# Optimization experiments

Measured on AMD Instinct MI355X. Metric: run time of the kernel, lower is better.

The kernel has to match this reference:

```python
import jax, jax.numpy as jnp
import numpy as np

B, C, D, L, H = 128, 1000, 300, 40, 100


def setup_inputs() -> dict:
    key = jax.random.key(0)
    ks = jax.random.split(key, 16)
    def rn(i, shape, sc=1.0):
        return (jax.random.normal(ks[i], shape, jnp.float32) * sc).astype(jnp.float32)
    return {
        "utt": rn(0, (B, L, D)),
        "sys_slots": rn(1, (B, D), 0.1),
        "conf_slots": rn(2, (B, D), 0.1),
        "conf_values": rn(3, (B, D), 0.1),
        "y_past_state": jax.random.uniform(ks[4], (B, C), jnp.float32),
        "slot_emb": rn(5, (C, D), 0.1),
        "value_emb": rn(6, (C, D), 0.1),
        "Wc": rn(7, (D, 2 * D), 0.05), "bc": jnp.zeros((D,), jnp.float32),
        "conv_w1": rn(8, (D, D, 1), 0.05), "conv_b1": jnp.zeros((D,), jnp.float32),
        "conv_w2": rn(9, (D, D, 2), 0.05), "conv_b2": jnp.zeros((D,), jnp.float32),
        "conv_w3": rn(10, (D, D, 3), 0.05), "conv_b3": jnp.zeros((D,), jnp.float32),
        "Wd": rn(11, (H, D), 0.05), "bd": jnp.zeros((H,), jnp.float32),
        "Wmr": rn(12, (H, D), 0.05), "bmr": jnp.zeros((H,), jnp.float32),
        "Wmc": rn(13, (H, D), 0.05), "bmc": jnp.zeros((H,), jnp.float32),
        "Wj": rn(14, (1, H), 0.05), "bj": jnp.zeros((1,), jnp.float32),
    }


def _conv_relu_pool(x_ncl, w, b):
    # x_ncl: [B, D, L]; w: [F, D, k] -> relu(conv) then global max-pool over time -> [B, F]
    y = jax.lax.conv_general_dilated(x_ncl, w, (1,), 'VALID',
                                     dimension_numbers=('NCH', 'OIH', 'NCH'))
    y = jax.nn.relu(y + b[None, :, None])
    return jnp.max(y, axis=2)


def _sig_linear(x, W, b):
    # Sequential(Sigmoid, Linear): Linear applied to sigmoid(x)
    return jax.nn.sigmoid(x) @ W.T + b


def reference(utt, sys_slots, conf_slots, conf_values, y_past_state,
              slot_emb, value_emb, Wc, bc,
              conv_w1, conv_b1, conv_w2, conv_b2, conv_w3, conv_b3,
              Wd, bd, Wmr, bmr, Wmc, bmc, Wj, bj):
    # CNN utterance encoder: sum of 3 conv branches (filter widths 1,2,3)
    x = jnp.transpose(utt, (0, 2, 1))  # [B, D, L]
    final_utt = (_conv_relu_pool(x, conv_w1, conv_b1)
                 + _conv_relu_pool(x, conv_w2, conv_b2)
                 + _conv_relu_pool(x, conv_w3, conv_b3))  # [B, D]

    # candidates_transform = sigmoid(Linear(cat(slot_emb, value_emb)))
    cand = jax.nn.sigmoid(jnp.concatenate([slot_emb, value_emb], axis=1) @ Wc.T + bc)  # [C, D]

    # fused version of the per-batch repeat/addcmul loop: [B, C, D]
    contrib = cand[None, :, :] * final_utt[:, None, :]

    y1 = _sig_linear(_sig_linear(contrib, Wd, bd), Wj, bj)  # [B, C, 1]

    # system-act request gate: ([C,D]@[D,B]) @ [B,D] -> [C, D]
    m_r = (slot_emb @ sys_slots.T) @ final_utt
    y2 = _sig_linear(_sig_linear(m_r, Wmr, bmr), Wj, bj)  # [C, 1]

    # system-act confirm gate
    m_c = ((slot_emb @ conf_slots.T) * (value_emb @ conf_values.T)) @ final_utt  # [C, D]
    y3 = _sig_linear(_sig_linear(m_c, Wmc, bmc), Wj, bj)  # [C, 1]

    y_presoftmax = y1 + y2[None, :, :] + y3[None, :, :]  # [B, C, 1]
    combine = 0.5
    return combine * y_presoftmax[..., 0] + (1.0 - combine) * y_past_state  # [B, C]
```

## Files before the change

### kernel.cpp

```cpp
#include <hip/hip_runtime.h>
#include <hip/hip_bf16.h>

#define OFF_Y23     0
#define OFF_BDP     4096
#define OFF_WJP     4544
#define OFF_BCP     4992
#define OFF_BMRP    6272
#define OFF_BMCP    6720
#define OFF_WALLT   7168
#define OFF_PBF     1235968
#define OFF_FUBF    20896768
#define OFF_FUBFT   20978688
#define OFF_CATSV   21060608
#define OFF_WCPK    22371328
#define OFF_CANDBF  22780928
#define OFF_WDFRAG  23436288
#define OFF_WMRFRAG 23507968
#define OFF_WMCFRAG 23579648
#define OFF_SYSB    23651328
#define OFF_CONFSB  23733248
#define OFF_CONFVB  23815168
#define OFF_PRBF    23897088
#define OFF_PCBF    24159232
#define OFF_SMRBF   24421376
#define OFF_SMCBF   25076736
#define OFF_XBF     25732096

typedef short bf16x8_t __attribute__((ext_vector_type(8)));
typedef float f32x4_t  __attribute__((ext_vector_type(4)));

__device__ __forceinline__ float sigmoidf_fast(float x) {
    return __builtin_amdgcn_rcpf(1.0f + __expf(-x));
}
__device__ __forceinline__ unsigned short f2bf(float x) {
    unsigned int u = __float_as_uint(x);
    unsigned int r = (u + 0x7FFFu + ((u >> 16) & 1u)) >> 16;
    return (unsigned short)r;
}
__device__ __forceinline__ float bf2f(unsigned short h) {
    return __uint_as_float(((unsigned int)h) << 16);
}

__global__ __launch_bounds__(256) void pack_kernel(const float* __restrict__ w1,
        const float* __restrict__ w2, const float* __restrict__ w3,
        const float* __restrict__ Wc, const float* __restrict__ Wd,
        const float* __restrict__ Wmr, const float* __restrict__ Wmc,
        const float* __restrict__ sys, const float* __restrict__ confs,
        const float* __restrict__ confv, const float* __restrict__ bd,
        const float* __restrict__ Wj, const float* __restrict__ bmr,
        const float* __restrict__ bmc, const float* __restrict__ bc,
        const float* __restrict__ slot, const float* __restrict__ value,
        const float* __restrict__ utt,
        unsigned short* __restrict__ WallTbf, unsigned short* __restrict__ WdFrag,
        unsigned short* __restrict__ WmrFrag, unsigned short* __restrict__ WmcFrag,
        float* __restrict__ bdPad, float* __restrict__ WjPad,
        float* __restrict__ bmrPad, float* __restrict__ bmcPad,
        float* __restrict__ bcPad,
        unsigned short* __restrict__ sysB, unsigned short* __restrict__ confsB,
        unsigned short* __restrict__ confvB, unsigned short* __restrict__ catsv,
        unsigned short* __restrict__ WcPk, unsigned short* __restrict__ Xbf) {
    int t = blockIdx.x * 256 + threadIdx.x;
    union { unsigned short u[8]; uint4 q; } o;
    if (t < 76800) {
        int i8 = t * 8;
        int tap = i8 / 102400;
        int rem = i8 - tap * 102400;
        int f = rem / 320, k0 = rem % 320;
        #pragma unroll
        for (int e = 0; e < 8; e++) {
            int k = k0 + e;
            float v = 0.0f;
            if (f < 300 && k < 300) {
                int fd = f * 300 + k;
                v = (tap == 0) ? w1[fd] : (tap == 1) ? w2[fd * 2]
                  : (tap == 2) ? w2[fd * 2 + 1] : w3[fd * 3 + (tap - 3)];
            }
            o.u[e] = f2bf(v);
        }
        *(uint4*)(WallTbf + i8) = o.q;
    } else if (t < 90240) {
        int ent = t - 76800;
        int mat = ent / 4480;
        int le = ent - mat * 4480;
        const float* W = (mat == 0) ? Wd : ((mat == 1) ? Wmr : Wmc);
        unsigned short* dst = (mat == 0) ? WdFrag : ((mat == 1) ? WmrFrag : WmcFrag);
        int kt = le / 448;
        int r = le - kt * 448;
        int ni = r >> 6, lane = r & 63;
        int j = ni * 16 + (lane & 15);
        int kb = kt * 32 + (lane >> 4) * 8;
        #pragma unroll
        for (int e = 0; e < 8; e++) {
            int k = kb + e;
            o.u[e] = f2bf((j < 100 && k < 300) ? W[j * 300 + k] : 0.0f);
        }
        *(uint4*)(dst + le * 8) = o.q;
    } else if (t < 105600) {
        int i8 = (t - 90240) * 8;
        int m = i8 / 40960, r = i8 - m * 40960;
        int bb = r / 320, k0 = r % 320;
        const float* src = (m == 0) ? sys : ((m == 1) ? confs : confv);
        unsigned short* dst = (m == 0) ? sysB : ((m == 1) ? confsB : confvB);
        #pragma unroll
        for (int e = 0; e < 8; e++) {
            int k = k0 + e;
            o.u[e] = f2bf((k < 300) ? src[bb * 300 + k] : 0.0f);
        }
        *(uint4*)(dst + r) = o.q;
    } else if (t < 187520) {
        int i8 = (t - 105600) * 8;
        int c = i8 / 640, k0 = i8 % 640;
        #pragma unroll
        for (int e = 0; e < 8; e++) {
            int k = k0 + e;
            float v = 0.0f;
            if (c < 1000) {
                if (k < 300)                  v = slot[c * 300 + k];
                else if (k >= 320 && k < 620) v = value[c * 300 + (k - 320)];
            }
            o.u[e] = f2bf(v);
        }
        *(uint4*)(catsv + i8) = o.q;
    } else if (t < 213120) {
        int i8 = (t - 187520) * 8;
        int f = i8 / 640, k0 = i8 % 640;
        #pragma unroll
        for (int e = 0; e < 8; e++) {
            int k = k0 + e;
            float v = 0.0f;
            if (f < 300) {
                if (k < 300)                  v = Wc[f * 600 + k];
                else if (k >= 320 && k < 620) v = Wc[f * 600 + 300 + (k - 320)];
            }
            o.u[e] = f2bf(v);
        }
        *(uint4*)(WcPk + i8) = o.q;
    } else if (t < 417920) {
        int i8 = (t - 213120) * 8;
        int m = i8 / 320, k0 = i8 % 320;
        if (k0 + 8 <= 300) {
            float4 a = *(const float4*)(utt + m * 300 + k0);
            float4 b = *(const float4*)(utt + m * 300 + k0 + 4);
            o.u[0] = f2bf(a.x); o.u[1] = f2bf(a.y); o.u[2] = f2bf(a.z); o.u[3] = f2bf(a.w);
            o.u[4] = f2bf(b.x); o.u[5] = f2bf(b.y); o.u[6] = f2bf(b.z); o.u[7] = f2bf(b.w);
        } else {
            #pragma unroll
            for (int e = 0; e < 8; e++) {
                int k = k0 + e;
                o.u[e] = f2bf((k < 300) ? utt[m * 300 + k] : 0.0f);
            }
        }
        *(uint4*)(Xbf + i8) = o.q;
    } else if (t < 418688) {
        int j = t - 417920;
        if (j < 112)      bdPad[j] = (j < 100) ? bd[j] : 0.0f;
        else if (j < 224) { int jj = j - 112; WjPad[jj]  = (jj < 100) ? Wj[jj]  : 0.0f; }
        else if (j < 336) { int jj = j - 224; bmrPad[jj] = (jj < 100) ? bmr[jj] : 0.0f; }
        else if (j < 448) { int jj = j - 336; bmcPad[jj] = (jj < 100) ? bmc[jj] : 0.0f; }
        else              { int jj = j - 448; bcPad[jj]  = (jj < 300) ? bc[jj]  : 0.0f; }
    }
}

__global__ __launch_bounds__(256, 4) void early_kernel(
        const unsigned short* __restrict__ Xbf, const unsigned short* __restrict__ WallTbf,
        unsigned short* __restrict__ Pbf,
        const unsigned short* __restrict__ catsv, const unsigned short* __restrict__ WcPk,
        const float* __restrict__ bcPad, unsigned short* __restrict__ candbf,
        const unsigned short* __restrict__ sysB, const unsigned short* __restrict__ confsB,
        const unsigned short* __restrict__ confvB,
        unsigned short* __restrict__ Prbf, unsigned short* __restrict__ Pcbf) {
    __shared__ __attribute__((aligned(16))) char smem[25600];
    const int bid = blockIdx.x;
    const int tid = threadIdx.x;
    const int lane = tid & 63, w = tid >> 6;
    const int ln = lane & 15, lq = lane >> 4;

    if (bid >= 112) {
        short* As = (short*)smem;
        short* Bs = (short*)(smem + 5120);
        const int g = bid - 112;
        const int xcd = g & 7;
        const int idx2 = g >> 3;
        const int m0 = (xcd * 10 + idx2 / 15) * 64;
        const int n0 = (idx2 % 15) * 128;
        const int arow = tid >> 2, aq = tid & 3;
        f32x4_t acc[4][2];
        #pragma unroll
        for (int i = 0; i < 4; i++)
            #pragma unroll
            for (int j = 0; j < 2; j++) acc[i][j] = (f32x4_t){0.f, 0.f, 0.f, 0.f};

        const unsigned short* aSrc  = Xbf + (m0 + arow) * 320 + aq * 8;
        const unsigned short* bSrc0 = WallTbf + (n0 + arow) * 320 + aq * 8;
        const unsigned short* bSrc1 = WallTbf + (n0 + 64 + arow) * 320 + aq * 8;
        uint4 pa  = *(const uint4*)(aSrc);
        uint4 pb0 = *(const uint4*)(bSrc0);
        uint4 pb1 = *(const uint4*)(bSrc1);
        *(uint4*)(&As[arow * 40 + aq * 8]) = pa;
        *(uint4*)(&Bs[arow * 40 + aq * 8]) = pb0;
        *(uint4*)(&Bs[(64 + arow) * 40 + aq * 8]) = pb1;
        __syncthreads();

        #pragma unroll 1
        for (int kt = 0; kt < 10; kt++) {
            if (kt < 9) {
                int kk2 = (kt + 1) * 32;
                pa  = *(const uint4*)(aSrc + kk2);
                pb0 = *(const uint4*)(bSrc0 + kk2);
                pb1 = *(const uint4*)(bSrc1 + kk2);
            }
            bf16x8_t a[4], b[2];
            #pragma unroll
            for (int mi = 0; mi < 4; mi++)
                a[mi] = *(const bf16x8_t*)(&As[(mi * 16 + ln) * 40 + lq * 8]);
            #pragma unroll
            for (int ni = 0; ni < 2; ni++)
                b[ni] = *(const bf16x8_t*)(&Bs[(w * 32 + ni * 16 + ln) * 40 + lq * 8]);
            #pragma unroll
            for (int mi = 0; mi < 4; mi++)
                #pragma unroll
                for (int ni = 0; ni < 2; ni++)
                    acc[mi][ni] = __builtin_amdgcn_mfma_f32_16x16x32_bf16(a[mi], b[ni], acc[mi][ni], 0, 0, 0);
            if (kt < 9) {
                __syncthreads();
                *(uint4*)(&As[arow * 40 + aq * 8]) = pa;
                *(uint4*)(&Bs[arow * 40 + aq * 8]) = pb0;
                *(uint4*)(&Bs[(64 + arow) * 40 + aq * 8]) = pb1;
                __syncthreads();
            }
        }
        #pragma unroll
        for (int mi = 0; mi < 4; mi++) {
            #pragma unroll
            for (int ni = 0; ni < 2; ni++) {
                int col = n0 + w * 32 + ni * 16 + ln;
                #pragma unroll
                for (int reg = 0; reg < 4; reg++) {
                    int row = m0 + mi * 16 + lq * 4 + reg;
                    Pbf[row * 1920 + col] = f2bf(acc[mi][ni][reg]);
                }
            }
        }
    } else if (bid < 80) {
        short* As = (short*)smem;
        short* Bs = (short*)(smem + 5120);
        const int m0 = (bid / 5) * 64, n0 = (bid % 5) * 64;
        const int wr = w & 1, wc = w >> 1;
        f32x4_t acc[2][2];
        #pragma unroll
        for (int i = 0; i < 2; i++)
            #pragma unroll
            for (int j = 0; j < 2; j++) acc[i][j] = (f32x4_t){0.f, 0.f, 0.f, 0.f};
        const int srow = tid >> 2, sq = tid & 3;
        for (int kk = 0; kk < 640; kk += 32) {
            *(uint4*)(&As[srow * 40 + sq * 8]) = *(const uint4*)(catsv + (m0 + srow) * 640 + kk + sq * 8);
            *(uint4*)(&Bs[srow * 40 + sq * 8]) = *(const uint4*)(WcPk  + (n0 + srow) * 640 + kk + sq * 8);
            __syncthreads();
            bf16x8_t a[2], b[2];
            #pragma unroll
            for (int mi = 0; mi < 2; mi++)
                a[mi] = *(const bf16x8_t*)(&As[(wr * 32 + mi * 16 + ln) * 40 + lq * 8]);
            #pragma unroll
            for (int ni = 0; ni < 2; ni++)
                b[ni] = *(const bf16x8_t*)(&Bs[(wc * 32 + ni * 16 + ln) * 40 + lq * 8]);
            #pragma unroll
            for (int mi = 0; mi < 2; mi++)
                #pragma unroll
                for (int ni = 0; ni < 2; ni++)
                    acc[mi][ni] = __builtin_amdgcn_mfma_f32_16x16x32_bf16(a[mi], b[ni], acc[mi][ni], 0, 0, 0);
            __syncthreads();
        }
        #pragma unroll
        for (int mi = 0; mi < 2; mi++) {
            #pragma unroll
            for (int ni = 0; ni < 2; ni++) {
                int n = n0 + wc * 32 + ni * 16 + ln;
                float bcv = bcPad[n];
                #pragma unroll
                for (int reg = 0; reg < 4; reg++) {
                    int cr = m0 + wr * 32 + mi * 16 + lq * 4 + reg;
                    candbf[cr * 320 + n] = f2bf(sigmoidf_fast(acc[mi][ni][reg] + bcv));
                }
            }
        }
    } else {
        short* As0 = (short*)smem;
        short* As1 = (short*)(smem + 5120);
        short* Bs0 = (short*)(smem + 10240);
        short* Bs1 = (short*)(smem + 15360);
        short* Bs2 = (short*)(smem + 20480);
        const int pid = bid - 80;
        const int c0 = (pid >> 1) * 64;
        const int bh = (pid & 1) * 64;
        f32x4_t accR[4], accS[4], accV[4];
        #pragma unroll
        for (int i = 0; i < 4; i++) {
            accR[i] = (f32x4_t){0.f, 0.f, 0.f, 0.f};
            accS[i] = (f32x4_t){0.f, 0.f, 0.f, 0.f};
            accV[i] = (f32x4_t){0.f, 0.f, 0.f, 0.f};
        }
        for (int kk = 0; kk < 320; kk += 32) {
            #pragma unroll
            for (int i = tid; i < 512; i += 256) {
                int mat = i >> 8, r2 = i & 255;
                int row = r2 >> 2, q = r2 & 3;
                short* dst = mat ? As1 : As0;
                *(uint4*)(&dst[row * 40 + q * 8]) =
                    *(const uint4*)(catsv + (c0 + row) * 640 + mat * 320 + kk + q * 8);
            }
            #pragma unroll
            for (int i = tid; i < 768; i += 256) {
                int mat = i >> 8, r2 = i & 255;
                int row = r2 >> 2, q = r2 & 3;
                const unsigned short* src = (mat == 0) ? sysB : ((mat == 1) ? confsB : confvB);
                short* dst = (mat == 0) ? Bs0 : ((mat == 1) ? Bs1 : Bs2);
                *(uint4*)(&dst[row * 40 + q * 8]) =
                    *(const uint4*)(src + (bh + row) * 320 + kk + q * 8);
            }
            __syncthreads();
            bf16x8_t aS = *(const bf16x8_t*)(&As0[(w * 16 + ln) * 40 + lq * 8]);
            bf16x8_t aV = *(const bf16x8_t*)(&As1[(w * 16 + ln) * 40 + lq * 8]);
            #pragma unroll
            for (int ni = 0; ni < 4; ni++) {
                bf16x8_t bR = *(const bf16x8_t*)(&Bs0[(ni * 16 + ln) * 40 + lq * 8]);
                bf16x8_t bS = *(const bf16x8_t*)(&Bs1[(ni * 16 + ln) * 40 + lq * 8]);
                bf16x8_t bV = *(const bf16x8_t*)(&Bs2[(ni * 16 + ln) * 40 + lq * 8]);
                accR[ni] = __builtin_amdgcn_mfma_f32_16x16x32_bf16(aS, bR, accR[ni], 0, 0, 0);
                accS[ni] = __builtin_amdgcn_mfma_f32_16x16x32_bf16(aS, bS, accS[ni], 0, 0, 0);
                accV[ni] = __builtin_amdgcn_mfma_f32_16x16x32_bf16(aV, bV, accV[ni], 0, 0, 0);
            }
            __syncthreads();
        }
        #pragma unroll
        for (int ni = 0; ni < 4; ni++) {
            int b = bh + ni * 16 + ln;
            #pragma unroll
            for (int reg = 0; reg < 4; reg++) {
                int c = c0 + w * 16 + lq * 4 + reg;
                Prbf[c * 128 + b] = f2bf(accR[ni][reg]);
                Pcbf[c * 128 + b] = f2bf(accS[ni][reg] * accV[ni][reg]);
            }
        }
    }
}

__global__ __launch_bounds__(64) void combine_kernel(const unsigned short* __restrict__ Pbf,
        const float* __restrict__ b1, const float* __restrict__ b2,
        const float* __restrict__ b3, unsigned short* __restrict__ fubf,
        unsigned short* __restrict__ fubfT) {
    int b = blockIdx.x;
    int f = blockIdx.y * 64 + threadIdx.x;
    if (f >= 300) { fubf[b * 320 + f] = 0; fubfT[f * 128 + b] = 0; return; }
    const unsigned short* base = Pbf + (size_t)b * 40 * 1920;
    float m1 = -1e30f, m2 = -1e30f, m3 = -1e30f;
    float p1prev = 0.f, p3prev = 0.f, p3prev2 = 0.f, p4prev = 0.f;
    for (int t = 0; t < 40; ++t) {
        const unsigned short* r = base + t * 1920;
        float p0 = bf2f(r[f]);
        float p1 = bf2f(r[320 + f]);
        float p2 = bf2f(r[640 + f]);
        float p3 = bf2f(r[960 + f]);
        float p4 = bf2f(r[1280 + f]);
        float p5 = bf2f(r[1600 + f]);
        m1 = fmaxf(m1, p0);
        if (t >= 1) m2 = fmaxf(m2, p1prev + p2);
        if (t >= 2) m3 = fmaxf(m3, p3prev2 + p4prev + p5);
        p3prev2 = p3prev; p3prev = p3; p4prev = p4; p1prev = p1;
    }
    float r = fmaxf(m1 + b1[f], 0.f) + fmaxf(m2 + b2[f], 0.f) + fmaxf(m3 + b3[f], 0.f);
    unsigned short rb = f2bf(r);
    fubf[b * 320 + f]  = rb;
    fubfT[f * 128 + b] = rb;
}

__global__ __launch_bounds__(256) void mgate_gemm(const unsigned short* __restrict__ Prbf,
        const unsigned short* __restrict__ Pcbf, const unsigned short* __restrict__ fubfT,
        unsigned short* __restrict__ smrbf, unsigned short* __restrict__ smcbf) {
    __shared__ __attribute__((aligned(16))) short As[2][64 * 40];
    __shared__ __attribute__((aligned(16))) short Bs[64 * 40];
    const int tid = threadIdx.x;
    const int m0 = blockIdx.x * 64, n0 = blockIdx.y * 64;
    const int lane = tid & 63, w = tid >> 6;
    const int wr = w & 1, wc = w >> 1;
    const int ln = lane & 15, lq = lane >> 4;
    f32x4_t accR[2][2], accC[2][2];
    #pragma unroll
    for (int i = 0; i < 2; i++)
        #pragma unroll
        for (int j = 0; j < 2; j++) {
            accR[i][j] = (f32x4_t){0.f, 0.f, 0.f, 0.f};
            accC[i][j] = (f32x4_t){0.f, 0.f, 0.f, 0.f};
        }
    for (int kk = 0; kk < 128; kk += 32) {
        #pragma unroll
        for (int i = tid; i < 512; i += 256) {
            int mat = i >> 8, r2 = i & 255;
            int row = r2 >> 2, q = r2 & 3;
            const unsigned short* src = mat ? Pcbf : Prbf;
            *(uint4*)(&As[mat][row * 40 + q * 8]) =
                *(const uint4*)(src + (m0 + row) * 128 + kk + q * 8);
        }
        if (tid < 256) {
            int row = tid >> 2, q = tid & 3;
            *(uint4*)(&Bs[row * 40 + q * 8]) =
                *(const uint4*)(fubfT + (n0 + row) * 128 + kk + q * 8);
        }
        __syncthreads();
        bf16x8_t aR[2], aC[2], b[2];
        #pragma unroll
        for (int mi = 0; mi < 2; mi++) {
            aR[mi] = *(const bf16x8_t*)(&As[0][(wr * 32 + mi * 16 + ln) * 40 + lq * 8]);
            aC[mi] = *(const bf16x8_t*)(&As[1][(wr * 32 + mi * 16 + ln) * 40 + lq * 8]);
        }
        #pragma unroll
        for (int ni = 0; ni < 2; ni++)
            b[ni] = *(const bf16x8_t*)(&Bs[(wc * 32 + ni * 16 + ln) * 40 + lq * 8]);
        #pragma unroll
        for (int mi = 0; mi < 2; mi++)
            #pragma unroll
            for (int ni = 0; ni < 2; ni++) {
                accR[mi][ni] = __builtin_amdgcn_mfma_f32_16x16x32_bf16(aR[mi], b[ni], accR[mi][ni], 0, 0, 0);
                accC[mi][ni] = __builtin_amdgcn_mfma_f32_16x16x32_bf16(aC[mi], b[ni], accC[mi][ni], 0, 0, 0);
            }
        __syncthreads();
    }
    #pragma unroll
    for (int mi = 0; mi < 2; mi++) {
        #pragma unroll
        for (int ni = 0; ni < 2; ni++) {
            int f = n0 + wc * 32 + ni * 16 + ln;
            #pragma unroll
            for (int reg = 0; reg < 4; reg++) {
                int c = m0 + wr * 32 + mi * 16 + lq * 4 + reg;
                smrbf[c * 320 + f] = f2bf(sigmoidf_fast(accR[mi][ni][reg]));
                smcbf[c * 320 + f] = f2bf(sigmoidf_fast(accC[mi][ni][reg]));
            }
        }
    }
}

__global__ __launch_bounds__(256) void ygate_gemm(const unsigned short* __restrict__ smrbf,
        const unsigned short* __restrict__ smcbf, const unsigned short* __restrict__ WmrFrag,
        const unsigned short* __restrict__ WmcFrag, const float* __restrict__ bmrPad,
        const float* __restrict__ bmcPad, const float* __restrict__ WjPad,
        const float* __restrict__ bj, float* __restrict__ y23) {
    __shared__ __attribute__((aligned(16))) short As[2][64 * 40];
    __shared__ __attribute__((aligned(16))) short Bs[2][3584];
    const int tid = threadIdx.x;
    const int c0 = blockIdx.x * 64;
    const int lane = tid & 63, w = tid >> 6;
    const int ln = lane & 15, lq = lane >> 4;
    f32x4_t accR[7], accC[7];
    #pragma unroll
    for (int i = 0; i < 7; i++) {
        accR[i] = (f32x4_t){0.f, 0.f, 0.f, 0.f};
        accC[i] = (f32x4_t){0.f, 0.f, 0.f, 0.f};
    }
    for (int kt = 0; kt < 10; kt++) {
        int kk = kt * 32;
        #pragma unroll
        for (int i = tid; i < 512; i += 256) {
            int mat = i >> 8, r2 = i & 255;
            int row = r2 >> 2, q = r2 & 3;
            const unsigned short* src = mat ? smcbf : smrbf;
            *(uint4*)(&As[mat][row * 40 + q * 8]) =
                *(const uint4*)(src + (c0 + row) * 320 + kk + q * 8);
        }
        #pragma unroll
        for (int i = tid; i < 896; i += 256) {
            int mat = i / 448, j = i - mat * 448;
            const uint4* s = (const uint4*)((mat ? WmcFrag : WmrFrag) + kt * 3584);
            ((uint4*)&Bs[mat][0])[j] = s[j];
        }
        __syncthreads();
        bf16x8_t aR = *(const bf16x8_t*)(&As[0][(w * 16 + ln) * 40 + lq * 8]);
        bf16x8_t aC = *(const bf16x8_t*)(&As[1][(w * 16 + ln) * 40 + lq * 8]);
        #pragma unroll
        for (int ni = 0; ni < 7; ni++) {
            bf16x8_t bR = *(const bf16x8_t*)(&Bs[0][(ni * 64 + lane) * 8]);
            bf16x8_t bC = *(const bf16x8_t*)(&Bs[1][(ni * 64 + lane) * 8]);
            accR[ni] = __builtin_amdgcn_mfma_f32_16x16x32_bf16(aR, bR, accR[ni], 0, 0, 0);
            accC[ni] = __builtin_amdgcn_mfma_f32_16x16x32_bf16(aC, bC, accC[ni], 0, 0, 0);
        }
        __syncthreads();
    }
    float psum[4] = {0.f, 0.f, 0.f, 0.f};
    #pragma unroll
    for (int ni = 0; ni < 7; ni++) {
        int n = ni * 16 + ln;
        float wj = WjPad[n], br = bmrPad[n], bcv = bmcPad[n];
        #pragma unroll
        for (int reg = 0; reg < 4; reg++) {
            float hr = sigmoidf_fast(accR[ni][reg] + br);
            float hc = sigmoidf_fast(accC[ni][reg] + bcv);
            psum[reg] += (hr + hc) * wj;
        }
    }
    #pragma unroll
    for (int reg = 0; reg < 4; reg++) {
        float v = psum[reg];
        v += __shfl_xor(v, 1);
        v += __shfl_xor(v, 2);
        v += __shfl_xor(v, 4);
        v += __shfl_xor(v, 8);
        if (ln == 0) {
            int c = c0 + w * 16 + lq * 4 + reg;
            y23[c] = v + 2.0f * bj[0];
        }
    }
}

__global__ __launch_bounds__(256) void gemm2_kernel(const unsigned short* __restrict__ candbf,
        const unsigned short* __restrict__ fubf, const unsigned short* __restrict__ WdFrag,
        const float* __restrict__ bdPad, const float* __restrict__ WjPad,
        const float* __restrict__ bj, const float* __restrict__ y23,
        const float* __restrict__ ypast, float* __restrict__ out) {
    __shared__ __attribute__((aligned(16))) short Bs[2][3584];
    __shared__ float bdS[112], WjS[112], ybuf[128];
    const int c = blockIdx.x;
    const int tid = threadIdx.x;
    const int lane = tid & 63, w = tid >> 6;
    const int ln = lane & 15, lq = lane >> 4;
    if (tid < 112) { bdS[tid] = bdPad[tid]; WjS[tid] = WjPad[tid]; }

    const unsigned short* candRow = candbf + c * 320;
    const unsigned short* fuR0 = fubf + (w * 32 + ln) * 320;
    const unsigned short* fuR1 = fuR0 + 16 * 320;

    f32x4_t acc[2][7];
    #pragma unroll
    for (int mi = 0; mi < 2; mi++)
        #pragma unroll
        for (int ni = 0; ni < 7; ni++) acc[mi][ni] = (f32x4_t){0.f, 0.f, 0.f, 0.f};

    {
        const uint4* src = (const uint4*)(WdFrag);
        uint4* dst = (uint4*)&Bs[0][0];
        dst[tid] = src[tid];
        if (tid < 192) dst[tid + 256] = src[tid + 256];
    }
    __syncthreads();

    #pragma unroll
    for (int kt = 0; kt < 10; kt++) {
        if (kt < 9) {
            const uint4* src = (const uint4*)(WdFrag + (kt + 1) * 3584);
            uint4* dst = (uint4*)&Bs[(kt + 1) & 1][0];
            dst[tid] = src[tid];
            if (tid < 192) dst[tid + 256] = src[tid + 256];
        }
        const int k0 = kt * 32 + lq * 8;
        bf16x8_t cf  = *(const bf16x8_t*)(candRow + k0);
        bf16x8_t f0v = *(const bf16x8_t*)(fuR0 + k0);
        bf16x8_t f1v = *(const bf16x8_t*)(fuR1 + k0);
        bf16x8_t a0, a1;
        #pragma unroll
        for (int e = 0; e < 8; e += 2) {
            float cv0 = bf2f((unsigned short)cf[e]);
            float cv1 = bf2f((unsigned short)cf[e + 1]);
            float2 s0 = make_float2(sigmoidf_fast(cv0 * bf2f((unsigned short)f0v[e])),
                                    sigmoidf_fast(cv1 * bf2f((unsigned short)f0v[e + 1])));
            float2 s1 = make_float2(sigmoidf_fast(cv0 * bf2f((unsigned short)f1v[e])),
                                    sigmoidf_fast(cv1 * bf2f((unsigned short)f1v[e + 1])));
            __hip_bfloat162 p0 = __float22bfloat162_rn(s0);
            __hip_bfloat162 p1 = __float22bfloat162_rn(s1);
            ((unsigned int*)&a0)[e >> 1] = *(unsigned int*)&p0;
            ((unsigned int*)&a1)[e >> 1] = *(unsigned int*)&p1;
        }
        #pragma unroll
        for (int ni = 0; ni < 7; ni++) {
            bf16x8_t bfr = *(const bf16x8_t*)(&Bs[kt & 1][(ni * 64 + lane) * 8]);
            acc[0][ni] = __builtin_amdgcn_mfma_f32_16x16x32_bf16(a0, bfr, acc[0][ni], 0, 0, 0);
            acc[1][ni] = __builtin_amdgcn_mfma_f32_16x16x32_bf16(a1, bfr, acc[1][ni], 0, 0, 0);
        }
        __syncthreads();
    }

    float psum[2][4] = {{0.f, 0.f, 0.f, 0.f}, {0.f, 0.f, 0.f, 0.f}};
    #pragma unroll
    for (int mi = 0; mi < 2; mi++) {
        #pragma unroll
        for (int ni = 0; ni < 7; ni++) {
            int n = ni * 16 + ln;
            float bdv = bdS[n], wjv = WjS[n];
            #pragma unroll
            for (int reg = 0; reg < 4; reg++) {
                float h = sigmoidf_fast(acc[mi][ni][reg] + bdv);
                psum[mi][reg] += h * wjv;
            }
        }
    }
    #pragma unroll
    for (int mi = 0; mi < 2; mi++) {
        #pragma unroll
        for (int reg = 0; reg < 4; reg++) {
            float v = psum[mi][reg];
            v += __shfl_xor(v, 1);
            v += __shfl_xor(v, 2);
            v += __shfl_xor(v, 4);
            v += __shfl_xor(v, 8);
            if (ln == 0) ybuf[w * 32 + mi * 16 + lq * 4 + reg] = v;
        }
    }
    __syncthreads();
    if (tid < 128) {
        int b = tid;
        float y1 = ybuf[b] + bj[0];
        out[b * 1000 + c] = 0.5f * (y1 + y23[c]) + 0.5f * ypast[b * 1000 + c];
    }
}

extern "C" void kernel_launch(void* const* d_in, const int* in_sizes, int n_in,
                              void* d_out, int out_size, void* d_ws, size_t ws_size,
                              hipStream_t stream) {
    const float* utt   = (const float*)d_in[0];
    const float* sys   = (const float*)d_in[1];
    const float* confs = (const float*)d_in[2];
    const float* confv = (const float*)d_in[3];
    const float* ypast = (const float*)d_in[4];
    const float* slot  = (const float*)d_in[5];
    const float* value = (const float*)d_in[6];
    const float* Wc    = (const float*)d_in[7];
    const float* bc    = (const float*)d_in[8];
    const float* w1    = (const float*)d_in[9];
    const float* b1    = (const float*)d_in[10];
    const float* w2    = (const float*)d_in[11];
    const float* b2    = (const float*)d_in[12];
    const float* w3    = (const float*)d_in[13];
    const float* b3    = (const float*)d_in[14];
    const float* Wd    = (const float*)d_in[15];
    const float* bd    = (const float*)d_in[16];
    const float* Wmr   = (const float*)d_in[17];
    const float* bmr   = (const float*)d_in[18];
    const float* Wmc   = (const float*)d_in[19];
    const float* bmc   = (const float*)d_in[20];
    const float* Wj    = (const float*)d_in[21];
    const float* bj    = (const float*)d_in[22];

    char* wsb = (char*)d_ws;
    float* y23    = (float*)(wsb + OFF_Y23);
    float* bdPad  = (float*)(wsb + OFF_BDP);
    float* WjPad  = (float*)(wsb + OFF_WJP);
    float* bcPad  = (float*)(wsb + OFF_BCP);
    float* bmrPad = (float*)(wsb + OFF_BMRP);
    float* bmcPad = (float*)(wsb + OFF_BMCP);
    unsigned short* WallTbf = (unsigned short*)(wsb + OFF_WALLT);
    unsigned short* Pbf     = (unsigned short*)(wsb + OFF_PBF);
    unsigned short* fubf    = (unsigned short*)(wsb + OFF_FUBF);
    unsigned short* fubfT   = (unsigned short*)(wsb + OFF_FUBFT);
    unsigned short* catsv   = (unsigned short*)(wsb + OFF_CATSV);
    unsigned short* WcPk    = (unsigned short*)(wsb + OFF_WCPK);
    unsigned short* candbf  = (unsigned short*)(wsb + OFF_CANDBF);
    unsigned short* WdFrag  = (unsigned short*)(wsb + OFF_WDFRAG);
    unsigned short* WmrFrag = (unsigned short*)(wsb + OFF_WMRFRAG);
    unsigned short* WmcFrag = (unsigned short*)(wsb + OFF_WMCFRAG);
    unsigned short* sysB    = (unsigned short*)(wsb + OFF_SYSB);
    unsigned short* confsB  = (unsigned short*)(wsb + OFF_CONFSB);
    unsigned short* confvB  = (unsigned short*)(wsb + OFF_CONFVB);
    unsigned short* Prbf    = (unsigned short*)(wsb + OFF_PRBF);
    unsigned short* Pcbf    = (unsigned short*)(wsb + OFF_PCBF);
    unsigned short* smrbf   = (unsigned short*)(wsb + OFF_SMRBF);
    unsigned short* smcbf   = (unsigned short*)(wsb + OFF_SMCBF);
    unsigned short* Xbf     = (unsigned short*)(wsb + OFF_XBF);
    float* out = (float*)d_out;

    pack_kernel<<<1636, 256, 0, stream>>>(w1, w2, w3, Wc, Wd, Wmr, Wmc, sys, confs, confv,
                                          bd, Wj, bmr, bmc, bc, slot, value, utt,
                                          WallTbf, WdFrag, WmrFrag, WmcFrag,
                                          bdPad, WjPad, bmrPad, bmcPad, bcPad,
                                          sysB, confsB, confvB, catsv, WcPk, Xbf);
    early_kernel<<<1312, 256, 0, stream>>>(Xbf, WallTbf, Pbf,
                                           catsv, WcPk, bcPad, candbf,
                                           sysB, confsB, confvB, Prbf, Pcbf);
    combine_kernel<<<dim3(128, 5), 64, 0, stream>>>(Pbf, b1, b2, b3, fubf, fubfT);
    mgate_gemm<<<dim3(16, 5), 256, 0, stream>>>(Prbf, Pcbf, fubfT, smrbf, smcbf);
    ygate_gemm<<<16, 256, 0, stream>>>(smrbf, smcbf, WmrFrag, WmcFrag,
                                       bmrPad, bmcPad, WjPad, bj, y23);
    gemm2_kernel<<<1000, 256, 0, stream>>>(candbf, fubf, WdFrag, bdPad, WjPad,
                                           bj, y23, ypast, out);
}
```

Baseline: 191.5 us.

## Load MFMA operands directly from global memory, dropping LDS staging and barriers

In three GEMM kernels (mgate_gemm, ygate_gemm, gemm2_kernel), the shared-memory staging of A/B tiles is removed and each lane loads its bf16x8 MFMA fragments straight from global memory, relying on L1/L2 caching. All __syncthreads in the k-loops go away, and gemm2 gets a launch_bounds occupancy hint of 4 plus partial unrolling. This removes LDS copy traffic and barrier stalls, but can raise global/L2 load traffic, since tiles are no longer shared across waves, and exposes load latency without explicit double-buffering.

```diff
diff --git a/kernel.cpp b/kernel.cpp
--- a/kernel.cpp
+++ b/kernel.cpp
@@ -376,8 +376,6 @@
 __global__ __launch_bounds__(256) void mgate_gemm(const unsigned short* __restrict__ Prbf,
         const unsigned short* __restrict__ Pcbf, const unsigned short* __restrict__ fubfT,
         unsigned short* __restrict__ smrbf, unsigned short* __restrict__ smcbf) {
-    __shared__ __attribute__((aligned(16))) short As[2][64 * 40];
-    __shared__ __attribute__((aligned(16))) short Bs[64 * 40];
     const int tid = threadIdx.x;
     const int m0 = blockIdx.x * 64, n0 = blockIdx.y * 64;
     const int lane = tid & 63, w = tid >> 6;
@@ -391,30 +389,18 @@
             accR[i][j] = (f32x4_t){0.f, 0.f, 0.f, 0.f};
             accC[i][j] = (f32x4_t){0.f, 0.f, 0.f, 0.f};
         }
+    #pragma unroll
     for (int kk = 0; kk < 128; kk += 32) {
-        #pragma unroll
-        for (int i = tid; i < 512; i += 256) {
-            int mat = i >> 8, r2 = i & 255;
-            int row = r2 >> 2, q = r2 & 3;
-            const unsigned short* src = mat ? Pcbf : Prbf;
-            *(uint4*)(&As[mat][row * 40 + q * 8]) =
-                *(const uint4*)(src + (m0 + row) * 128 + kk + q * 8);
-        }
-        if (tid < 256) {
-            int row = tid >> 2, q = tid & 3;
-            *(uint4*)(&Bs[row * 40 + q * 8]) =
-                *(const uint4*)(fubfT + (n0 + row) * 128 + kk + q * 8);
-        }
-        __syncthreads();
         bf16x8_t aR[2], aC[2], b[2];
         #pragma unroll
         for (int mi = 0; mi < 2; mi++) {
-            aR[mi] = *(const bf16x8_t*)(&As[0][(wr * 32 + mi * 16 + ln) * 40 + lq * 8]);
-            aC[mi] = *(const bf16x8_t*)(&As[1][(wr * 32 + mi * 16 + ln) * 40 + lq * 8]);
+            int row = m0 + wr * 32 + mi * 16 + ln;
+            aR[mi] = *(const bf16x8_t*)(Prbf + row * 128 + kk + lq * 8);
+            aC[mi] = *(const bf16x8_t*)(Pcbf + row * 128 + kk + lq * 8);
         }
         #pragma unroll
         for (int ni = 0; ni < 2; ni++)
-            b[ni] = *(const bf16x8_t*)(&Bs[(wc * 32 + ni * 16 + ln) * 40 + lq * 8]);
+            b[ni] = *(const bf16x8_t*)(fubfT + (n0 + wc * 32 + ni * 16 + ln) * 128 + kk + lq * 8);
         #pragma unroll
         for (int mi = 0; mi < 2; mi++)
             #pragma unroll
@@ -422,7 +408,6 @@
                 accR[mi][ni] = __builtin_amdgcn_mfma_f32_16x16x32_bf16(aR[mi], b[ni], accR[mi][ni], 0, 0, 0);
                 accC[mi][ni] = __builtin_amdgcn_mfma_f32_16x16x32_bf16(aC[mi], b[ni], accC[mi][ni], 0, 0, 0);
             }
-        __syncthreads();
     }
     #pragma unroll
     for (int mi = 0; mi < 2; mi++) {
@@ -444,8 +429,6 @@
         const unsigned short* __restrict__ WmcFrag, const float* __restrict__ bmrPad,
         const float* __restrict__ bmcPad, const float* __restrict__ WjPad,
         const float* __restrict__ bj, float* __restrict__ y23) {
-    __shared__ __attribute__((aligned(16))) short As[2][64 * 40];
-    __shared__ __attribute__((aligned(16))) short Bs[2][3584];
     const int tid = threadIdx.x;
     const int c0 = blockIdx.x * 64;
     const int lane = tid & 63, w = tid >> 6;
@@ -456,33 +439,19 @@
         accR[i] = (f32x4_t){0.f, 0.f, 0.f, 0.f};
         accC[i] = (f32x4_t){0.f, 0.f, 0.f, 0.f};
     }
+    const int arow = (c0 + w * 16 + ln) * 320 + lq * 8;
+    const int bbase = lane * 8;
+    #pragma unroll 2
     for (int kt = 0; kt < 10; kt++) {
-        int kk = kt * 32;
-        #pragma unroll
-        for (int i = tid; i < 512; i += 256) {
-            int mat = i >> 8, r2 = i & 255;
-            int row = r2 >> 2, q = r2 & 3;
-            const unsigned short* src = mat ? smcbf : smrbf;
-            *(uint4*)(&As[mat][row * 40 + q * 8]) =
-                *(const uint4*)(src + (c0 + row) * 320 + kk + q * 8);
-        }
-        #pragma unroll
-        for (int i = tid; i < 896; i += 256) {
-            int mat = i / 448, j = i - mat * 448;
-            const uint4* s = (const uint4*)((mat ? WmcFrag : WmrFrag) + kt * 3584);
-            ((uint4*)&Bs[mat][0])[j] = s[j];
-        }
-        __syncthreads();
-        bf16x8_t aR = *(const bf16x8_t*)(&As[0][(w * 16 + ln) * 40 + lq * 8]);
-        bf16x8_t aC = *(const bf16x8_t*)(&As[1][(w * 16 + ln) * 40 + lq * 8]);
+        bf16x8_t aR = *(const bf16x8_t*)(smrbf + arow + kt * 32);
+        bf16x8_t aC = *(const bf16x8_t*)(smcbf + arow + kt * 32);
         #pragma unroll
         for (int ni = 0; ni < 7; ni++) {
-            bf16x8_t bR = *(const bf16x8_t*)(&Bs[0][(ni * 64 + lane) * 8]);
-            bf16x8_t bC = *(const bf16x8_t*)(&Bs[1][(ni * 64 + lane) * 8]);
+            bf16x8_t bR = *(const bf16x8_t*)(WmrFrag + kt * 3584 + ni * 512 + bbase);
+            bf16x8_t bC = *(const bf16x8_t*)(WmcFrag + kt * 3584 + ni * 512 + bbase);
             accR[ni] = __builtin_amdgcn_mfma_f32_16x16x32_bf16(aR, bR, accR[ni], 0, 0, 0);
             accC[ni] = __builtin_amdgcn_mfma_f32_16x16x32_bf16(aC, bC, accC[ni], 0, 0, 0);
         }
-        __syncthreads();
     }
     float psum[4] = {0.f, 0.f, 0.f, 0.f};
     #pragma unroll
@@ -510,22 +479,21 @@
     }
 }
 
-__global__ __launch_bounds__(256) void gemm2_kernel(const unsigned short* __restrict__ candbf,
+__global__ __launch_bounds__(256, 4) void gemm2_kernel(const unsigned short* __restrict__ candbf,
         const unsigned short* __restrict__ fubf, const unsigned short* __restrict__ WdFrag,
         const float* __restrict__ bdPad, const float* __restrict__ WjPad,
         const float* __restrict__ bj, const float* __restrict__ y23,
         const float* __restrict__ ypast, float* __restrict__ out) {
-    __shared__ __attribute__((aligned(16))) short Bs[2][3584];
-    __shared__ float bdS[112], WjS[112], ybuf[128];
+    __shared__ float ybuf[128];
     const int c = blockIdx.x;
     const int tid = threadIdx.x;
     const int lane = tid & 63, w = tid >> 6;
     const int ln = lane & 15, lq = lane >> 4;
-    if (tid < 112) { bdS[tid] = bdPad[tid]; WjS[tid] = WjPad[tid]; }
 
     const unsigned short* candRow = candbf + c * 320;
     const unsigned short* fuR0 = fubf + (w * 32 + ln) * 320;
     const unsigned short* fuR1 = fuR0 + 16 * 320;
+    const unsigned short* bBase = WdFrag + lane * 8;
 
     f32x4_t acc[2][7];
     #pragma unroll
@@ -533,22 +501,8 @@
         #pragma unroll
         for (int ni = 0; ni < 7; ni++) acc[mi][ni] = (f32x4_t){0.f, 0.f, 0.f, 0.f};
 
-    {
-        const uint4* src = (const uint4*)(WdFrag);
-        uint4* dst = (uint4*)&Bs[0][0];
-        dst[tid] = src[tid];
-        if (tid < 192) dst[tid + 256] = src[tid + 256];
-    }
-    __syncthreads();
-
-    #pragma unroll
+    #pragma unroll 2
     for (int kt = 0; kt < 10; kt++) {
-        if (kt < 9) {
-            const uint4* src = (const uint4*)(WdFrag + (kt + 1) * 3584);
-            uint4* dst = (uint4*)&Bs[(kt + 1) & 1][0];
-            dst[tid] = src[tid];
-            if (tid < 192) dst[tid + 256] = src[tid + 256];
-        }
         const int k0 = kt * 32 + lq * 8;
         bf16x8_t cf  = *(const bf16x8_t*)(candRow + k0);
         bf16x8_t f0v = *(const bf16x8_t*)(fuR0 + k0);
@@ -567,13 +521,13 @@
             ((unsigned int*)&a0)[e >> 1] = *(unsigned int*)&p0;
             ((unsigned int*)&a1)[e >> 1] = *(unsigned int*)&p1;
         }
+        const unsigned short* bkt = bBase + kt * 3584;
         #pragma unroll
         for (int ni = 0; ni < 7; ni++) {
-            bf16x8_t bfr = *(const bf16x8_t*)(&Bs[kt & 1][(ni * 64 + lane) * 8]);
+            bf16x8_t bfr = *(const bf16x8_t*)(bkt + ni * 512);
             acc[0][ni] = __builtin_amdgcn_mfma_f32_16x16x32_bf16(a0, bfr, acc[0][ni], 0, 0, 0);
             acc[1][ni] = __builtin_amdgcn_mfma_f32_16x16x32_bf16(a1, bfr, acc[1][ni], 0, 0, 0);
         }
-        __syncthreads();
     }
 
     float psum[2][4] = {{0.f, 0.f, 0.f, 0.f}, {0.f, 0.f, 0.f, 0.f}};
@@ -582,7 +536,7 @@
         #pragma unroll
         for (int ni = 0; ni < 7; ni++) {
             int n = ni * 16 + ln;
-            float bdv = bdS[n], wjv = WjS[n];
+            float bdv = bdPad[n], wjv = WjPad[n];
             #pragma unroll
             for (int reg = 0; reg < 4; reg++) {
                 float h = sigmoidf_fast(acc[mi][ni][reg] + bdv);
```

Result: slower. 195.7 us (+2.2%).

## Fuse combine, m-gate and y-gate kernels into one launch with atomic-counter handoffs

Applied to the files above, without the earlier changes.

Merges the pooling/combine kernel, the m-gate GEMM and the y-gate GEMM into a single 256-block kernel. Block ranges take the roles of the three stages and hand off through global atomic counters with spin-waits, and the counters are zeroed in the pack kernel. The aim is to remove two kernel launches and the idle gaps between small, low-occupancy stages. In exchange the correctness of the spin-waits depends on all 256 blocks being co-resident, which holds on a 256-CU device but is not guaranteed. Waiting blocks occupy CUs while they spin.

```diff
diff --git a/kernel.cpp b/kernel.cpp
--- a/kernel.cpp
+++ b/kernel.cpp
@@ -25,6 +25,7 @@
 #define OFF_SMRBF   24421376
 #define OFF_SMCBF   25076736
 #define OFF_XBF     25732096
+#define OFF_CNT     29008896
 
 typedef short bf16x8_t __attribute__((ext_vector_type(8)));
 typedef float f32x4_t  __attribute__((ext_vector_type(4)));
@@ -58,7 +59,8 @@
         float* __restrict__ bcPad,
         unsigned short* __restrict__ sysB, unsigned short* __restrict__ confsB,
         unsigned short* __restrict__ confvB, unsigned short* __restrict__ catsv,
-        unsigned short* __restrict__ WcPk, unsigned short* __restrict__ Xbf) {
+        unsigned short* __restrict__ WcPk, unsigned short* __restrict__ Xbf,
+        unsigned int* __restrict__ cnt) {
     int t = blockIdx.x * 256 + threadIdx.x;
     union { unsigned short u[8]; uint4 q; } o;
     if (t < 76800) {
@@ -158,6 +160,8 @@
         else if (j < 336) { int jj = j - 224; bmrPad[jj] = (jj < 100) ? bmr[jj] : 0.0f; }
         else if (j < 448) { int jj = j - 336; bmcPad[jj] = (jj < 100) ? bmc[jj] : 0.0f; }
         else              { int jj = j - 448; bcPad[jj]  = (jj < 300) ? bc[jj]  : 0.0f; }
+    } else if (t < 418690) {
+        cnt[t - 418688] = 0u;
     }
 }
 
@@ -344,168 +348,193 @@
     }
 }
 
-__global__ __launch_bounds__(64) void combine_kernel(const unsigned short* __restrict__ Pbf,
+__global__ __launch_bounds__(256) void tail_kernel(const unsigned short* __restrict__ Pbf,
         const float* __restrict__ b1, const float* __restrict__ b2,
         const float* __restrict__ b3, unsigned short* __restrict__ fubf,
-        unsigned short* __restrict__ fubfT) {
-    int b = blockIdx.x;
-    int f = blockIdx.y * 64 + threadIdx.x;
-    if (f >= 300) { fubf[b * 320 + f] = 0; fubfT[f * 128 + b] = 0; return; }
-    const unsigned short* base = Pbf + (size_t)b * 40 * 1920;
-    float m1 = -1e30f, m2 = -1e30f, m3 = -1e30f;
-    float p1prev = 0.f, p3prev = 0.f, p3prev2 = 0.f, p4prev = 0.f;
-    for (int t = 0; t < 40; ++t) {
-        const unsigned short* r = base + t * 1920;
-        float p0 = bf2f(r[f]);
-        float p1 = bf2f(r[320 + f]);
-        float p2 = bf2f(r[640 + f]);
-        float p3 = bf2f(r[960 + f]);
-        float p4 = bf2f(r[1280 + f]);
-        float p5 = bf2f(r[1600 + f]);
-        m1 = fmaxf(m1, p0);
-        if (t >= 1) m2 = fmaxf(m2, p1prev + p2);
-        if (t >= 2) m3 = fmaxf(m3, p3prev2 + p4prev + p5);
-        p3prev2 = p3prev; p3prev = p3; p4prev = p4; p1prev = p1;
-    }
-    float r = fmaxf(m1 + b1[f], 0.f) + fmaxf(m2 + b2[f], 0.f) + fmaxf(m3 + b3[f], 0.f);
-    unsigned short rb = f2bf(r);
-    fubf[b * 320 + f]  = rb;
-    fubfT[f * 128 + b] = rb;
-}
-
-__global__ __launch_bounds__(256) void mgate_gemm(const unsigned short* __restrict__ Prbf,
-        const unsigned short* __restrict__ Pcbf, const unsigned short* __restrict__ fubfT,
-        unsigned short* __restrict__ smrbf, unsigned short* __restrict__ smcbf) {
-    __shared__ __attribute__((aligned(16))) short As[2][64 * 40];
-    __shared__ __attribute__((aligned(16))) short Bs[64 * 40];
+        unsigned short* __restrict__ fubfT,
+        const unsigned short* __restrict__ Prbf, const unsigned short* __restrict__ Pcbf,
+        unsigned short* __restrict__ smrbf, unsigned short* __restrict__ smcbf,
+        const unsigned short* __restrict__ WmrFrag, const unsigned short* __restrict__ WmcFrag,
+        const float* __restrict__ bmrPad, const float* __restrict__ bmcPad,
+        const float* __restrict__ WjPad, const float* __restrict__ bj,
+        float* __restrict__ y23, unsigned int* __restrict__ cnt) {
+    __shared__ __attribute__((aligned(16))) char smem[24576];
+    const int bid = blockIdx.x;
     const int tid = threadIdx.x;
-    const int m0 = blockIdx.x * 64, n0 = blockIdx.y * 64;
-    const int lane = tid & 63, w = tid >> 6;
-    const int wr = w & 1, wc = w >> 1;
-    const int ln = lane & 15, lq = lane >> 4;
-    f32x4_t accR[2][2], accC[2][2];
-    #pragma unroll
-    for (int i = 0; i < 2; i++)
-        #pragma unroll
-        for (int j = 0; j < 2; j++) {
-            accR[i][j] = (f32x4_t){0.f, 0.f, 0.f, 0.f};
-            accC[i][j] = (f32x4_t){0.f, 0.f, 0.f, 0.f};
-        }
-    for (int kk = 0; kk < 128; kk += 32) {
-        #pragma unroll
-        for (int i = tid; i < 512; i += 256) {
-            int mat = i >> 8, r2 = i & 255;
-            int row = r2 >> 2, q = r2 & 3;
-            const unsigned short* src = mat ? Pcbf : Prbf;
-            *(uint4*)(&As[mat][row * 40 + q * 8]) =
-                *(const uint4*)(src + (m0 + row) * 128 + kk + q * 8);
-        }
-        if (tid < 256) {
-            int row = tid >> 2, q = tid & 3;
-            *(uint4*)(&Bs[row * 40 + q * 8]) =
-                *(const uint4*)(fubfT + (n0 + row) * 128 + kk + q * 8);
-        }
-        __syncthreads();
-        bf16x8_t aR[2], aC[2], b[2];
-        #pragma unroll
-        for (int mi = 0; mi < 2; mi++) {
-            aR[mi] = *(const bf16x8_t*)(&As[0][(wr * 32 + mi * 16 + ln) * 40 + lq * 8]);
-            aC[mi] = *(const bf16x8_t*)(&As[1][(wr * 32 + mi * 16 + ln) * 40 + lq * 8]);
-        }
-        #pragma unroll
-        for (int ni = 0; ni < 2; ni++)
-            b[ni] = *(const bf16x8_t*)(&Bs[(wc * 32 + ni * 16 + ln) * 40 + lq * 8]);
-        #pragma unroll
-        for (int mi = 0; mi < 2; mi++)
-            #pragma unroll
-            for (int ni = 0; ni < 2; ni++) {
-                accR[mi][ni] = __builtin_amdgcn_mfma_f32_16x16x32_bf16(aR[mi], b[ni], accR[mi][ni], 0, 0, 0);
-                accC[mi][ni] = __builtin_amdgcn_mfma_f32_16x16x32_bf16(aC[mi], b[ni], accC[mi][ni], 0, 0, 0);
-            }
-        __syncthreads();
-    }
-    #pragma unroll
-    for (int mi = 0; mi < 2; mi++) {
-        #pragma unroll
-        for (int ni = 0; ni < 2; ni++) {
-            int f = n0 + wc * 32 + ni * 16 + ln;
-            #pragma unroll
-            for (int reg = 0; reg < 4; reg++) {
-                int c = m0 + wr * 32 + mi * 16 + lq * 4 + reg;
-                smrbf[c * 320 + f] = f2bf(sigmoidf_fast(accR[mi][ni][reg]));
-                smcbf[c * 320 + f] = f2bf(sigmoidf_fast(accC[mi][ni][reg]));
-            }
-        }
-    }
-}
-
-__global__ __launch_bounds__(256) void ygate_gemm(const unsigned short* __restrict__ smrbf,
-        const unsigned short* __restrict__ smcbf, const unsigned short* __restrict__ WmrFrag,
-        const unsigned short* __restrict__ WmcFrag, const float* __restrict__ bmrPad,
-        const float* __restrict__ bmcPad, const float* __restrict__ WjPad,
-        const float* __restrict__ bj, float* __restrict__ y23) {
-    __shared__ __attribute__((aligned(16))) short As[2][64 * 40];
-    __shared__ __attribute__((aligned(16))) short Bs[2][3584];
-    const int tid = threadIdx.x;
-    const int c0 = blockIdx.x * 64;
     const int lane = tid & 63, w = tid >> 6;
     const int ln = lane & 15, lq = lane >> 4;
-    f32x4_t accR[7], accC[7];
-    #pragma unroll
-    for (int i = 0; i < 7; i++) {
-        accR[i] = (f32x4_t){0.f, 0.f, 0.f, 0.f};
-        accC[i] = (f32x4_t){0.f, 0.f, 0.f, 0.f};
-    }
-    for (int kt = 0; kt < 10; kt++) {
-        int kk = kt * 32;
-        #pragma unroll
-        for (int i = tid; i < 512; i += 256) {
-            int mat = i >> 8, r2 = i & 255;
-            int row = r2 >> 2, q = r2 & 3;
-            const unsigned short* src = mat ? smcbf : smrbf;
-            *(uint4*)(&As[mat][row * 40 + q * 8]) =
-                *(const uint4*)(src + (c0 + row) * 320 + kk + q * 8);
-        }
-        #pragma unroll
-        for (int i = tid; i < 896; i += 256) {
-            int mat = i / 448, j = i - mat * 448;
-            const uint4* s = (const uint4*)((mat ? WmcFrag : WmrFrag) + kt * 3584);
-            ((uint4*)&Bs[mat][0])[j] = s[j];
-        }
+
+    if (bid < 160) {
+        int g = bid * 256 + tid;
+        int b = g / 320, f = g % 320;
+        if (f >= 300) {
+            fubf[b * 320 + f] = 0; fubfT[f * 128 + b] = 0;
+        } else {
+            const unsigned short* base = Pbf + (size_t)b * 40 * 1920;
+            float m1 = -1e30f, m2 = -1e30f, m3 = -1e30f;
+            float p1prev = 0.f, p3prev = 0.f, p3prev2 = 0.f, p4prev = 0.f;
+            for (int t = 0; t < 40; ++t) {
+                const unsigned short* r = base + t * 1920;
+                float p0 = bf2f(r[f]);
+                float p1 = bf2f(r[320 + f]);
+                float p2 = bf2f(r[640 + f]);
+                float p3 = bf2f(r[960 + f]);
+                float p4 = bf2f(r[1280 + f]);
+                float p5 = bf2f(r[1600 + f]);
+                m1 = fmaxf(m1, p0);
+                if (t >= 1) m2 = fmaxf(m2, p1prev + p2);
+                if (t >= 2) m3 = fmaxf(m3, p3prev2 + p4prev + p5);
+                p3prev2 = p3prev; p3prev = p3; p4prev = p4; p1prev = p1;
+            }
+            float r = fmaxf(m1 + b1[f], 0.f) + fmaxf(m2 + b2[f], 0.f) + fmaxf(m3 + b3[f], 0.f);
+            unsigned short rb = f2bf(r);
+            fubf[b * 320 + f]  = rb;
+            fubfT[f * 128 + b] = rb;
+        }
+        __threadfence();
         __syncthreads();
-        bf16x8_t aR = *(const bf16x8_t*)(&As[0][(w * 16 + ln) * 40 + lq * 8]);
-        bf16x8_t aC = *(const bf16x8_t*)(&As[1][(w * 16 + ln) * 40 + lq * 8]);
+        if (tid == 0) atomicAdd(&cnt[0], 1u);
+    } else if (bid < 240) {
+        if (tid == 0) {
+            while (__hip_atomic_load(&cnt[0], __ATOMIC_RELAXED, __HIP_MEMORY_SCOPE_AGENT) < 160u)
+                __builtin_amdgcn_s_sleep(8);
+            __threadfence();
+        }
+        __syncthreads();
+        short* As0 = (short*)smem;
+        short* As1 = (short*)(smem + 5120);
+        short* Bs  = (short*)(smem + 10240);
+        const int pid = bid - 160;
+        const int m0 = (pid / 5) * 64, n0 = (pid % 5) * 64;
+        const int wr = w & 1, wc = w >> 1;
+        f32x4_t accR[2][2], accC[2][2];
+        #pragma unroll
+        for (int i = 0; i < 2; i++)
+            #pragma unroll
+            for (int j = 0; j < 2; j++) {
+                accR[i][j] = (f32x4_t){0.f, 0.f, 0.f, 0.f};
+                accC[i][j] = (f32x4_t){0.f, 0.f, 0.f, 0.f};
+            }
+        for (int kk = 0; kk < 128; kk += 32) {
+            #pragma unroll
+            for (int i = tid; i < 512; i += 256) {
+                int mat = i >> 8, r2 = i & 255;
+                int row = r2 >> 2, q = r2 & 3;
+                const unsigned short* src = mat ? Pcbf : Prbf;
+                short* dst = mat ? As1 : As0;
+                *(uint4*)(&dst[row * 40 + q * 8]) =
+                    *(const uint4*)(src + (m0 + row) * 128 + kk + q * 8);
+            }
+            {
+                int row = tid >> 2, q = tid & 3;
+                *(uint4*)(&Bs[row * 40 + q * 8]) =
+                    *(const uint4*)(fubfT + (n0 + row) * 128 + kk + q * 8);
+            }
+            __syncthreads();
+            bf16x8_t aR[2], aC[2], b[2];
+            #pragma unroll
+            for (int mi = 0; mi < 2; mi++) {
+                aR[mi] = *(const bf16x8_t*)(&As0[(wr * 32 + mi * 16 + ln) * 40 + lq * 8]);
+                aC[mi] = *(const bf16x8_t*)(&As1[(wr * 32 + mi * 16 + ln) * 40 + lq * 8]);
+            }
+            #pragma unroll
+            for (int ni = 0; ni < 2; ni++)
+                b[ni] = *(const bf16x8_t*)(&Bs[(wc * 32 + ni * 16 + ln) * 40 + lq * 8]);
+            #pragma unroll
+            for (int mi = 0; mi < 2; mi++)
+                #pragma unroll
+                for (int ni = 0; ni < 2; ni++) {
+                    accR[mi][ni] = __builtin_amdgcn_mfma_f32_16x16x32_bf16(aR[mi], b[ni], accR[mi][ni], 0, 0, 0);
+                    accC[mi][ni] = __builtin_amdgcn_mfma_f32_16x16x32_bf16(aC[mi], b[ni], accC[mi][ni], 0, 0, 0);
+                }
+            __syncthreads();
+        }
+        #pragma unroll
+        for (int mi = 0; mi < 2; mi++) {
+            #pragma unroll
+            for (int ni = 0; ni < 2; ni++) {
+                int f = n0 + wc * 32 + ni * 16 + ln;
+                #pragma unroll
+                for (int reg = 0; reg < 4; reg++) {
+                    int c = m0 + wr * 32 + mi * 16 + lq * 4 + reg;
+                    smrbf[c * 320 + f] = f2bf(sigmoidf_fast(accR[mi][ni][reg]));
+                    smcbf[c * 320 + f] = f2bf(sigmoidf_fast(accC[mi][ni][reg]));
+                }
+            }
+        }
+        __threadfence();
+        __syncthreads();
+        if (tid == 0) atomicAdd(&cnt[1], 1u);
+    } else {
+        if (tid == 0) {
+            while (__hip_atomic_load(&cnt[1], __ATOMIC_RELAXED, __HIP_MEMORY_SCOPE_AGENT) < 80u)
+                __builtin_amdgcn_s_sleep(8);
+            __threadfence();
+        }
+        __syncthreads();
+        short* As0 = (short*)smem;
+        short* As1 = (short*)(smem + 5120);
+        short* Bs0 = (short*)(smem + 10240);
+        short* Bs1 = (short*)(smem + 17408);
+        const int c0 = (bid - 240) * 64;
+        f32x4_t accR[7], accC[7];
+        #pragma unroll
+        for (int i = 0; i < 7; i++) {
+            accR[i] = (f32x4_t){0.f, 0.f, 0.f, 0.f};
+            accC[i] = (f32x4_t){0.f, 0.f, 0.f, 0.f};
+        }
+        for (int kt = 0; kt < 10; kt++) {
+            int kk = kt * 32;
+            #pragma unroll
+            for (int i = tid; i < 512; i += 256) {
+                int mat = i >> 8, r2 = i & 255;
+                int row = r2 >> 2, q = r2 & 3;
+                const unsigned short* src = mat ? smcbf : smrbf;
+                short* dst = mat ? As1 : As0;
+                *(uint4*)(&dst[row * 40 + q * 8]) =
+                    *(const uint4*)(src + (c0 + row) * 320 + kk + q * 8);
+            }
+            #pragma unroll
+            for (int i = tid; i < 896; i += 256) {
+                int mat = i / 448, j = i - mat * 448;
+                const uint4* s = (const uint4*)((mat ? WmcFrag : WmrFrag) + kt * 3584);
+                ((uint4*)(mat ? Bs1 : Bs0))[j] = s[j];
+            }
+            __syncthreads();
+            bf16x8_t aR = *(const bf16x8_t*)(&As0[(w * 16 + ln) * 40 + lq * 8]);
+            bf16x8_t aC = *(const bf16x8_t*)(&As1[(w * 16 + ln) * 40 + lq * 8]);
+            #pragma unroll
+            for (int ni = 0; ni < 7; ni++) {
+                bf16x8_t bR = *(const bf16x8_t*)(&Bs0[(ni * 64 + lane) * 8]);
+                bf16x8_t bC = *(const bf16x8_t*)(&Bs1[(ni * 64 + lane) * 8]);
+                accR[ni] = __builtin_amdgcn_mfma_f32_16x16x32_bf16(aR, bR, accR[ni], 0, 0, 0);
+                accC[ni] = __builtin_amdgcn_mfma_f32_16x16x32_bf16(aC, bC, accC[ni], 0, 0, 0);
+            }
+            __syncthreads();
+        }
+        float psum[4] = {0.f, 0.f, 0.f, 0.f};
         #pragma unroll
         for (int ni = 0; ni < 7; ni++) {
-            bf16x8_t bR = *(const bf16x8_t*)(&Bs[0][(ni * 64 + lane) * 8]);
-            bf16x8_t bC = *(const bf16x8_t*)(&Bs[1][(ni * 64 + lane) * 8]);
-            accR[ni] = __builtin_amdgcn_mfma_f32_16x16x32_bf16(aR, bR, accR[ni], 0, 0, 0);
-            accC[ni] = __builtin_amdgcn_mfma_f32_16x16x32_bf16(aC, bC, accC[ni], 0, 0, 0);
-        }
-        __syncthreads();
-    }
-    float psum[4] = {0.f, 0.f, 0.f, 0.f};
-    #pragma unroll
-    for (int ni = 0; ni < 7; ni++) {
-        int n = ni * 16 + ln;
-        float wj = WjPad[n], br = bmrPad[n], bcv = bmcPad[n];
+            int n = ni * 16 + ln;
+            float wj = WjPad[n], br = bmrPad[n], bcv = bmcPad[n];
+            #pragma unroll
+            for (int reg = 0; reg < 4; reg++) {
+                float hr = sigmoidf_fast(accR[ni][reg] + br);
+                float hc = sigmoidf_fast(accC[ni][reg] + bcv);
+                psum[reg] += (hr + hc) * wj;
+            }
+        }
         #pragma unroll
         for (int reg = 0; reg < 4; reg++) {
-            float hr = sigmoidf_fast(accR[ni][reg] + br);
-            float hc = sigmoidf_fast(accC[ni][reg] + bcv);
-            psum[reg] += (hr + hc) * wj;
-        }
-    }
-    #pragma unroll
-    for (int reg = 0; reg < 4; reg++) {
-        float v = psum[reg];
-        v += __shfl_xor(v, 1);
-        v += __shfl_xor(v, 2);
-        v += __shfl_xor(v, 4);
-        v += __shfl_xor(v, 8);
-        if (ln == 0) {
-            int c = c0 + w * 16 + lq * 4 + reg;
-            y23[c] = v + 2.0f * bj[0];
+            float v = psum[reg];
+            v += __shfl_xor(v, 1);
+            v += __shfl_xor(v, 2);
+            v += __shfl_xor(v, 4);
+            v += __shfl_xor(v, 8);
+            if (ln == 0) {
+                int c = c0 + w * 16 + lq * 4 + reg;
+                y23[c] = v + 2.0f * bj[0];
+            }
         }
     }
 }
@@ -662,20 +691,21 @@
     unsigned short* smrbf   = (unsigned short*)(wsb + OFF_SMRBF);
     unsigned short* smcbf   = (unsigned short*)(wsb + OFF_SMCBF);
     unsigned short* Xbf     = (unsigned short*)(wsb + OFF_XBF);
+    unsigned int*   cnt     = (unsigned int*)(wsb + OFF_CNT);
     float* out = (float*)d_out;
 
     pack_kernel<<<1636, 256, 0, stream>>>(w1, w2, w3, Wc, Wd, Wmr, Wmc, sys, confs, confv,
                                           bd, Wj, bmr, bmc, bc, slot, value, utt,
                                           WallTbf, WdFrag, WmrFrag, WmcFrag,
                                           bdPad, WjPad, bmrPad, bmcPad, bcPad,
-                                          sysB, confsB, confvB, catsv, WcPk, Xbf);
+                                          sysB, confsB, confvB, catsv, WcPk, Xbf, cnt);
     early_kernel<<<1312, 256, 0, stream>>>(Xbf, WallTbf, Pbf,
                                            catsv, WcPk, bcPad, candbf,
                                            sysB, confsB, confvB, Prbf, Pcbf);
-    combine_kernel<<<dim3(128, 5), 64, 0, stream>>>(Pbf, b1, b2, b3, fubf, fubfT);
-    mgate_gemm<<<dim3(16, 5), 256, 0, stream>>>(Prbf, Pcbf, fubfT, smrbf, smcbf);
-    ygate_gemm<<<16, 256, 0, stream>>>(smrbf, smcbf, WmrFrag, WmcFrag,
-                                       bmrPad, bmcPad, WjPad, bj, y23);
+    tail_kernel<<<256, 256, 0, stream>>>(Pbf, b1, b2, b3, fubf, fubfT,
+                                         Prbf, Pcbf, smrbf, smcbf,
+                                         WmrFrag, WmcFrag, bmrPad, bmcPad,
+                                         WjPad, bj, y23, cnt);
     gemm2_kernel<<<1000, 256, 0, stream>>>(candbf, fubf, WdFrag, bdPad, WjPad,
                                            bj, y23, ypast, out);
 }
```

Result: slower. 222.3 us (+16.1%).
